# Kernel optimization log

Hardware: AMD Instinct MI355X
Metric: run time of the kernel (lower is better)

Reference implementation:

```python
import jax, jax.numpy as jnp
import numpy as np

NEG_SLOPE = 0.01  # torch nn.LeakyReLU default

N_NODES = 100000
N_EDGES = 1000000
D_FEAT = 64


def setup_inputs() -> dict:
    key = jax.random.key(0)
    ks = jax.random.split(key, 8)
    x = jax.random.normal(ks[0], (N_NODES, D_FEAT), dtype=jnp.float32)
    src = jax.random.randint(ks[1], (N_EDGES,), 0, N_NODES, dtype=jnp.int64 if jax.config.jax_enable_x64 else jnp.int32)
    dst = jax.random.randint(ks[2], (N_EDGES,), 0, N_NODES, dtype=jnp.int64 if jax.config.jax_enable_x64 else jnp.int32)
    s = 1.0 / np.sqrt(D_FEAT)
    W1 = jax.random.normal(ks[3], (D_FEAT, 64), dtype=jnp.float32) * s
    b1 = jnp.zeros((64,), dtype=jnp.float32)
    W2 = jax.random.normal(ks[4], (64, 64), dtype=jnp.float32) * s
    b2 = jnp.zeros((64,), dtype=jnp.float32)
    Wc = jax.random.normal(ks[5], (64, 2), dtype=jnp.float32) * s
    bc = jnp.zeros((2,), dtype=jnp.float32)
    return {"x": x, "src": src, "dst": dst, "W1": W1, "b1": b1,
            "W2": W2, "b2": b2, "Wc": Wc, "bc": bc}


def _graph_conv(x, src, dst, W, b, out_deg_isqrt, in_deg_isqrt, n_nodes):
    # DGL GraphConv, norm='both': h_v = ( sum_{u->v} x_u / sqrt(d_out(u)) ) / sqrt(d_in(v)) @ W + b
    # (in_feats <= out_feats here, so aggregate first then transform, matching DGL order)
    h = x * out_deg_isqrt[:, None]          # [N, d] scale by source out-degree
    msg = h[src]                            # [E, d] gather
    agg = jax.ops.segment_sum(msg, dst, num_segments=n_nodes)  # [N, d] scatter-add
    agg = agg * in_deg_isqrt[:, None]
    return agg @ W + b


def reference(x, src, dst, W1, b1, W2, b2, Wc, bc):
    n = x.shape[0]
    ones_e = jnp.ones(src.shape[0], dtype=x.dtype)
    out_deg = jnp.clip(jax.ops.segment_sum(ones_e, src, num_segments=n), 1.0)
    in_deg = jnp.clip(jax.ops.segment_sum(ones_e, dst, num_segments=n), 1.0)
    out_isqrt = out_deg ** -0.5
    in_isqrt = in_deg ** -0.5

    h = _graph_conv(x, src, dst, W1, b1, out_isqrt, in_isqrt, n)
    h = jax.nn.leaky_relu(h, NEG_SLOPE)
    h = _graph_conv(h, src, dst, W2, b2, out_isqrt, in_isqrt, n)
    h = jax.nn.leaky_relu(h, NEG_SLOPE)
    return h @ Wc + bc  # prediction=True -> linear classifier
```

## Files before the change

### kernel.cpp

```cpp
#include <hip/hip_runtime.h>


typedef __attribute__((ext_vector_type(8))) short short8;
typedef __attribute__((ext_vector_type(4))) float f32x4;

#define NPB 256
#define SEG 64
#define BSH 9
#define BW  512

__device__ __forceinline__ float b2f(unsigned short u) {
    return __uint_as_float(((unsigned int)u) << 16);
}
__device__ __forceinline__ unsigned short f2b(float f) {
    unsigned int i = __float_as_uint(f);
    unsigned int r = (i + 0x7FFFu + ((i >> 16) & 1u)) >> 16;
    return (unsigned short)r;
}

__global__ __launch_bounds__(1024) void count_kernel(
    const int* __restrict__ src, const int* __restrict__ dst,
    int* __restrict__ cntD, int* __restrict__ cntS, int e, int chunk) {
    __shared__ int hD[256], hS[256];
    int t = threadIdx.x, pb = blockIdx.x;
    if (t < 256) { hD[t] = 0; hS[t] = 0; }
    __syncthreads();
    int e0 = pb * chunk, e1 = min(e, e0 + chunk);
    for (int i = e0 + 4 * t; i + 3 < e1; i += 4096) {
        int4 d4 = *(const int4*)(dst + i);
        int4 s4 = *(const int4*)(src + i);
        atomicAdd(&hD[d4.x >> BSH], 1);
        atomicAdd(&hD[d4.y >> BSH], 1);
        atomicAdd(&hD[d4.z >> BSH], 1);
        atomicAdd(&hD[d4.w >> BSH], 1);
        atomicAdd(&hS[s4.x >> BSH], 1);
        atomicAdd(&hS[s4.y >> BSH], 1);
        atomicAdd(&hS[s4.z >> BSH], 1);
        atomicAdd(&hS[s4.w >> BSH], 1);
    }
    int tb0 = e0 + ((e1 - e0) & ~3);
    for (int i = tb0 + t; i < e1; i += 1024) {
        atomicAdd(&hD[dst[i] >> BSH], 1);
        atomicAdd(&hS[src[i] >> BSH], 1);
    }
    __syncthreads();
    if (t < 256) {
        cntD[t * NPB + pb] = hD[t];
        cntS[t * NPB + pb] = hS[t];
    }
}

__global__ __launch_bounds__(1024) void scanmat_kernel(int* __restrict__ cntD,
                                                       int* __restrict__ cntS) {
    int* a = (blockIdx.x == 0) ? cntD : cntS;
    int4* a4 = (int4*)a;
    __shared__ int s[1024];
    int t = threadIdx.x;
    int4 v[SEG / 4];
    int sum = 0;
#pragma unroll
    for (int j = 0; j < SEG / 4; j++) {
        v[j] = a4[t * (SEG / 4) + j];
        sum += v[j].x + v[j].y + v[j].z + v[j].w;
    }
    s[t] = sum;
    __syncthreads();
    for (int d = 1; d < 1024; d <<= 1) {
        int x = (t >= d) ? s[t - d] : 0;
        __syncthreads();
        s[t] += x;
        __syncthreads();
    }
    int run = s[t] - sum;
#pragma unroll
    for (int j = 0; j < SEG / 4; j++) {
        int p0 = run;
        int p1 = p0 + v[j].x;
        int p2 = p1 + v[j].y;
        int p3 = p2 + v[j].z;
        run = p3 + v[j].w;
        a4[t * (SEG / 4) + j] = make_int4(p0, p1, p2, p3);
    }
}

__global__ __launch_bounds__(1024) void part_kernel(
    const int* __restrict__ src, const int* __restrict__ dst,
    const int* __restrict__ cntD, const int* __restrict__ cntS,
    unsigned int* __restrict__ ebuf, unsigned short* __restrict__ sbuf,
    int e, int chunk) {
    __shared__ int cD[256], cS[256];
    int t = threadIdx.x, pb = blockIdx.x;
    if (t < 256) {
        cD[t] = cntD[t * NPB + pb];
        cS[t] = cntS[t * NPB + pb];
    }
    __syncthreads();
    int e0 = pb * chunk, e1 = min(e, e0 + chunk);
    for (int i = e0 + 4 * t; i + 3 < e1; i += 4096) {
        int4 d4 = *(const int4*)(dst + i);
        int4 s4 = *(const int4*)(src + i);
#pragma unroll
        for (int k = 0; k < 4; k++) {
            int s_ = (k == 0) ? s4.x : (k == 1) ? s4.y : (k == 2) ? s4.z : s4.w;
            int d_ = (k == 0) ? d4.x : (k == 1) ? d4.y : (k == 2) ? d4.z : d4.w;
            int pd = atomicAdd(&cD[d_ >> BSH], 1);
            ebuf[pd] = ((unsigned int)s_ << BSH) | (unsigned int)(d_ & (BW - 1));
            int ps_ = atomicAdd(&cS[s_ >> BSH], 1);
            sbuf[ps_] = (unsigned short)(s_ & (BW - 1));
        }
    }
    int tb0 = e0 + ((e1 - e0) & ~3);
    for (int i = tb0 + t; i < e1; i += 1024) {
        int s_ = src[i], d_ = dst[i];
        int pd = atomicAdd(&cD[d_ >> BSH], 1);
        ebuf[pd] = ((unsigned int)s_ << BSH) | (unsigned int)(d_ & (BW - 1));
        int ps_ = atomicAdd(&cS[s_ >> BSH], 1);
        sbuf[ps_] = (unsigned short)(s_ & (BW - 1));
    }
}

__global__ __launch_bounds__(256) void bucket_kernel(
    const unsigned int* __restrict__ ebuf, const unsigned short* __restrict__ sbuf,
    const int* __restrict__ cntD, const int* __restrict__ cntS,
    int* __restrict__ row, float* __restrict__ ii, float* __restrict__ oi,
    int* __restrict__ csr, int n, int e) {
    __shared__ int cnt[BW], cur[BW], ocnt[BW], ps[256];
    int t = threadIdx.x, b = blockIdx.x;
    int v0 = b << BSH;
    int eb0 = cntD[b * NPB], eb1 = cntD[(b + 1) * NPB];
    int sb0 = cntS[b * NPB], sb1 = cntS[(b + 1) * NPB];
    cnt[t] = 0; cnt[t + 256] = 0;
    ocnt[t] = 0; ocnt[t + 256] = 0;
    __syncthreads();
    for (int i = eb0 + t; i < eb1; i += 256)
        atomicAdd(&cnt[ebuf[i] & (BW - 1)], 1);
    for (int i = sb0 + t; i < sb1; i += 256)
        atomicAdd(&ocnt[sbuf[i]], 1);
    __syncthreads();
    int c0 = cnt[2 * t], c1 = cnt[2 * t + 1];
    int pair = c0 + c1;
    ps[t] = pair;
    __syncthreads();
    for (int d = 1; d < 256; d <<= 1) {
        int x = (t >= d) ? ps[t - d] : 0;
        __syncthreads();
        ps[t] += x;
        __syncthreads();
    }
    int excl = ps[t] - pair;
    cur[2 * t] = excl;
    cur[2 * t + 1] = excl + c0;
    int v = v0 + 2 * t;
    if (v < n) {
        row[v] = eb0 + excl;
        ii[v] = rsqrtf((float)max(c0, 1));
    }
    if (v + 1 < n) {
        row[v + 1] = eb0 + excl + c0;
        ii[v + 1] = rsqrtf((float)max(c1, 1));
    }
    if (b == 0 && t == 0) row[n] = e;
    for (int j = t; j < BW; j += 256) {
        int vv = v0 + j;
        if (vv < n) oi[vv] = rsqrtf((float)max(ocnt[j], 1));
    }
    __syncthreads();
    for (int i = eb0 + t; i < eb1; i += 256) {
        unsigned int p = ebuf[i];
        int r = atomicAdd(&cur[p & (BW - 1)], 1);
        csr[eb0 + r] = (int)(p >> BSH);
    }
}

__global__ __launch_bounds__(256) void xconv_kernel(
    const float4* __restrict__ x4, const float* __restrict__ oi,
    ushort4* __restrict__ xb, int total4) {
    int stride = gridDim.x * blockDim.x;
    for (int i = blockIdx.x * blockDim.x + threadIdx.x; i < total4; i += stride) {
        float s = oi[i >> 4];
        float4 val = x4[i];
        xb[i] = make_ushort4(f2b(val.x * s), f2b(val.y * s),
                             f2b(val.z * s), f2b(val.w * s));
    }
}

template <bool FINAL>
__global__ __launch_bounds__(256) void fused_kernel(
    const short8* __restrict__ featb, const int* __restrict__ row,
    const int* __restrict__ csr, const float* __restrict__ ii,
    const float* __restrict__ oi,
    const float* __restrict__ W, const float* __restrict__ bias,
    const float* __restrict__ Wc, const float* __restrict__ bcl,
    void* __restrict__ out, int n, int nwaves) {
    __shared__ short8 tile[4][16 * 9];
    int lane = threadIdx.x & 63;
    int o = lane >> 3, s = lane & 7;
    int m15 = lane & 15, quad = lane >> 4;
    short8* tl = tile[threadIdx.x >> 6];
    int wid = blockIdx.x * (blockDim.x >> 6) + (threadIdx.x >> 6);
    int ngroups = (n + 15) >> 4;

    short8 bf[4][2];
#pragma unroll
    for (int nt = 0; nt < 4; nt++)
#pragma unroll
        for (int kk = 0; kk < 2; kk++)
#pragma unroll
            for (int j = 0; j < 8; j++)
                bf[nt][kk][j] = (short)f2b(W[(kk * 32 + quad * 8 + j) * 64 + nt * 16 + m15]);

    float bias_r[4];
#pragma unroll
    for (int nt = 0; nt < 4; nt++) bias_r[nt] = bias[nt * 16 + m15];

    float wc_r[4][2];
    float bc0 = 0.f, bc1 = 0.f;
    if constexpr (FINAL) {
#pragma unroll
        for (int nt = 0; nt < 4; nt++) {
            wc_r[nt][0] = Wc[(nt * 16 + m15) * 2];
            wc_r[nt][1] = Wc[(nt * 16 + m15) * 2 + 1];
        }
        bc0 = bcl[0];
        bc1 = bcl[1];
    }

    for (int g = wid; g < ngroups; g += nwaves) {
        int rbase = g << 4;

#pragma unroll
        for (int p = 0; p < 2; p++) {
            int v = rbase + p * 8 + o;
            bool valid = v < n;
            int base = 0, cnt = 0;
            if (valid) { base = row[v]; cnt = row[v + 1] - base; }
            float a[8];
#pragma unroll
            for (int k = 0; k < 8; k++) a[k] = 0.f;
            int j = 0;
            for (; j + 3 < cnt; j += 4) {
                int u[4];
#pragma unroll
                for (int k = 0; k < 4; k++) u[k] = csr[base + j + k];
#pragma unroll
                for (int k = 0; k < 4; k++) {
                    short8 f = featb[(size_t)u[k] * 8 + s];
#pragma unroll
                    for (int m = 0; m < 8; m++)
                        a[m] += b2f((unsigned short)f[m]);
                }
            }
            for (; j < cnt; j++) {
                short8 f = featb[(size_t)csr[base + j] * 8 + s];
#pragma unroll
                for (int m = 0; m < 8; m++)
                    a[m] += b2f((unsigned short)f[m]);
            }
            float iiv = valid ? ii[v] : 0.f;
            short8 r;
#pragma unroll
            for (int m = 0; m < 8; m++) r[m] = (short)f2b(a[m] * iiv);
            tl[(p * 8 + o) * 9 + s] = r;
        }

        short8 af0 = tl[m15 * 9 + quad];
        short8 af1 = tl[m15 * 9 + 4 + quad];

        f32x4 acc[4];
#pragma unroll
        for (int nt = 0; nt < 4; nt++) {
            f32x4 z = {0.f, 0.f, 0.f, 0.f};
            z = __builtin_amdgcn_mfma_f32_16x16x32_bf16(af0, bf[nt][0], z, 0, 0, 0);
            z = __builtin_amdgcn_mfma_f32_16x16x32_bf16(af1, bf[nt][1], z, 0, 0, 0);
            acc[nt] = z;
        }

        if constexpr (!FINAL) {
#pragma unroll
            for (int r = 0; r < 4; r++) {
                int vr = rbase + quad * 4 + r;
                float os = (vr < n) ? oi[vr] : 0.f;
#pragma unroll
                for (int nt = 0; nt < 4; nt++) {
                    float ov = acc[nt][r] + bias_r[nt];
                    ov = (ov > 0.f) ? ov : 0.01f * ov;
                    if (vr < n)
                        ((unsigned short*)out)[(size_t)vr * 64 + nt * 16 + m15] = f2b(ov * os);
                }
            }
        } else {
#pragma unroll
            for (int r = 0; r < 4; r++) {
                float p0 = 0.f, p1 = 0.f;
#pragma unroll
                for (int nt = 0; nt < 4; nt++) {
                    float ov = acc[nt][r] + bias_r[nt];
                    ov = (ov > 0.f) ? ov : 0.01f * ov;
                    p0 = fmaf(ov, wc_r[nt][0], p0);
                    p1 = fmaf(ov, wc_r[nt][1], p1);
                }
#pragma unroll
                for (int off = 1; off < 16; off <<= 1) {
                    p0 += __shfl_xor(p0, off);
                    p1 += __shfl_xor(p1, off);
                }
                int vr = rbase + quad * 4 + r;
                if (m15 == 0 && vr < n)
                    ((float2*)out)[vr] = make_float2(p0 + bc0, p1 + bc1);
            }
        }
    }
}

extern "C" void kernel_launch(void* const* d_in, const int* in_sizes, int n_in,
                              void* d_out, int out_size, void* d_ws, size_t ws_size,
                              hipStream_t stream) {
    const float* x  = (const float*)d_in[0];
    const int* src  = (const int*)d_in[1];
    const int* dst  = (const int*)d_in[2];
    const float* W1 = (const float*)d_in[3];
    const float* b1 = (const float*)d_in[4];
    const float* W2 = (const float*)d_in[5];
    const float* b2 = (const float*)d_in[6];
    const float* Wc = (const float*)d_in[7];
    const float* bc = (const float*)d_in[8];
    int n = in_sizes[0] / 64;
    int e = in_sizes[1];
    int total = n * 64;
    int nbuck = (n + BW - 1) >> BSH;

    char* ws = (char*)d_ws;
    size_t off = 0;
    auto take = [&](size_t bytes) -> char* {
        char* p = ws + off;
        off = (off + bytes + 255) & ~(size_t)255;
        return p;
    };
    int* cntD = (int*)take(256 * NPB * 4);
    int* cntS = (int*)take(256 * NPB * 4);
    unsigned int* ebuf = (unsigned int*)take((size_t)e * 4);
    unsigned short* sbuf = (unsigned short*)take((size_t)e * 2);
    int* row  = (int*)take((size_t)(n + 1) * 4);
    int* csr  = (int*)take((size_t)e * 4);
    float* oi = (float*)take((size_t)n * 4);
    float* ii = (float*)take((size_t)n * 4);
    unsigned short* xb  = (unsigned short*)take((size_t)total * 2);
    unsigned short* h1b = (unsigned short*)take((size_t)total * 2);

    int chunk = (((e + NPB - 1) / NPB) + 3) & ~3;

    count_kernel<<<NPB, 1024, 0, stream>>>(src, dst, cntD, cntS, e, chunk);
    scanmat_kernel<<<2, 1024, 0, stream>>>(cntD, cntS);
    part_kernel<<<NPB, 1024, 0, stream>>>(src, dst, cntD, cntS, ebuf, sbuf, e, chunk);
    bucket_kernel<<<nbuck, 256, 0, stream>>>(ebuf, sbuf, cntD, cntS,
                                             row, ii, oi, csr, n, e);
    xconv_kernel<<<2048, 256, 0, stream>>>((const float4*)x, oi, (ushort4*)xb,
                                           n * 16);

    const int fblocks = 1568;
    const int fwaves = fblocks * (256 / 64);

    fused_kernel<false><<<fblocks, 256, 0, stream>>>((const short8*)xb, row, csr, ii, oi,
                                                     W1, b1, nullptr, nullptr, h1b, n, fwaves);
    fused_kernel<true><<<fblocks, 256, 0, stream>>>((const short8*)h1b, row, csr, ii, nullptr,
                                                    W2, b2, Wc, bc, d_out, n, fwaves);
}
```

Before: 207.4 us.

## Pad CSR rows to multiples of four with a zero dummy node and vectorise the gather

Result: faster. 196.8 us (-5.1%).

```diff
diff --git a/kernel.cpp b/kernel.cpp
--- a/kernel.cpp
+++ b/kernel.cpp
@@ -16,6 +16,17 @@
     unsigned int i = __float_as_uint(f);
     unsigned int r = (i + 0x7FFFu + ((i >> 16) & 1u)) >> 16;
     return (unsigned short)r;
+}
+
+__device__ __forceinline__ void acc8(float* a, short8 f) {
+    int4 d = *(int4*)&f;
+#pragma unroll
+    for (int q = 0; q < 4; q++) {
+        unsigned int dw = (unsigned int)((q == 0) ? d.x : (q == 1) ? d.y
+                                       : (q == 2) ? d.z : d.w);
+        a[2 * q]     += __uint_as_float(dw << 16);
+        a[2 * q + 1] += __uint_as_float(dw & 0xFFFF0000u);
+    }
 }
 
 __global__ __launch_bounds__(1024) void count_kernel(
@@ -122,13 +133,15 @@
 __global__ __launch_bounds__(256) void bucket_kernel(
     const unsigned int* __restrict__ ebuf, const unsigned short* __restrict__ sbuf,
     const int* __restrict__ cntD, const int* __restrict__ cntS,
-    int* __restrict__ row, float* __restrict__ ii, float* __restrict__ oi,
+    int* __restrict__ row, int* __restrict__ lenp,
+    float* __restrict__ ii, float* __restrict__ oi,
     int* __restrict__ csr, int n, int e) {
     __shared__ int cnt[BW], cur[BW], ocnt[BW], ps[256];
     int t = threadIdx.x, b = blockIdx.x;
     int v0 = b << BSH;
     int eb0 = cntD[b * NPB], eb1 = cntD[(b + 1) * NPB];
     int sb0 = cntS[b * NPB], sb1 = cntS[(b + 1) * NPB];
+    int pbase = ((eb0 + 3) & ~3) + (v0 << 2);
     cnt[t] = 0; cnt[t + 256] = 0;
     ocnt[t] = 0; ocnt[t + 256] = 0;
     __syncthreads();
@@ -138,8 +151,9 @@
         atomicAdd(&ocnt[sbuf[i]], 1);
     __syncthreads();
     int c0 = cnt[2 * t], c1 = cnt[2 * t + 1];
-    int pair = c0 + c1;
-    ps[t] = pair;
+    int p0 = (c0 + 3) & ~3, p1 = (c1 + 3) & ~3;
+    int ppair = p0 + p1;
+    ps[t] = ppair;
     __syncthreads();
     for (int d = 1; d < 256; d <<= 1) {
         int x = (t >= d) ? ps[t - d] : 0;
@@ -147,19 +161,20 @@
         ps[t] += x;
         __syncthreads();
     }
-    int excl = ps[t] - pair;
-    cur[2 * t] = excl;
-    cur[2 * t + 1] = excl + c0;
+    int pexcl = ps[t] - ppair;
+    cur[2 * t] = pexcl;
+    cur[2 * t + 1] = pexcl + p0;
     int v = v0 + 2 * t;
     if (v < n) {
-        row[v] = eb0 + excl;
+        row[v] = pbase + pexcl;
+        lenp[v] = p0;
         ii[v] = rsqrtf((float)max(c0, 1));
     }
     if (v + 1 < n) {
-        row[v + 1] = eb0 + excl + c0;
+        row[v + 1] = pbase + pexcl + p0;
+        lenp[v + 1] = p1;
         ii[v + 1] = rsqrtf((float)max(c1, 1));
     }
-    if (b == 0 && t == 0) row[n] = e;
     for (int j = t; j < BW; j += 256) {
         int vv = v0 + j;
         if (vv < n) oi[vv] = rsqrtf((float)max(ocnt[j], 1));
@@ -168,27 +183,36 @@
     for (int i = eb0 + t; i < eb1; i += 256) {
         unsigned int p = ebuf[i];
         int r = atomicAdd(&cur[p & (BW - 1)], 1);
-        csr[eb0 + r] = (int)(p >> BSH);
-    }
+        csr[pbase + r] = (int)(p >> BSH);
+    }
+    if (v < n)
+        for (int k = c0; k < p0; k++) csr[pbase + pexcl + k] = n;
+    if (v + 1 < n)
+        for (int k = c1; k < p1; k++) csr[pbase + pexcl + p0 + k] = n;
 }
 
 __global__ __launch_bounds__(256) void xconv_kernel(
     const float4* __restrict__ x4, const float* __restrict__ oi,
-    ushort4* __restrict__ xb, int total4) {
+    ushort4* __restrict__ xb, ushort4* __restrict__ h1b4, int total4) {
+    int idx = blockIdx.x * blockDim.x + threadIdx.x;
     int stride = gridDim.x * blockDim.x;
-    for (int i = blockIdx.x * blockDim.x + threadIdx.x; i < total4; i += stride) {
+    for (int i = idx; i < total4; i += stride) {
         float s = oi[i >> 4];
         float4 val = x4[i];
         xb[i] = make_ushort4(f2b(val.x * s), f2b(val.y * s),
                              f2b(val.z * s), f2b(val.w * s));
     }
+    if (idx < 16) {
+        xb[total4 + idx] = make_ushort4(0, 0, 0, 0);
+        h1b4[total4 + idx] = make_ushort4(0, 0, 0, 0);
+    }
 }
 
 template <bool FINAL>
 __global__ __launch_bounds__(256) void fused_kernel(
     const short8* __restrict__ featb, const int* __restrict__ row,
-    const int* __restrict__ csr, const float* __restrict__ ii,
-    const float* __restrict__ oi,
+    const int* __restrict__ lenp, const int* __restrict__ csr,
+    const float* __restrict__ ii, const float* __restrict__ oi,
     const float* __restrict__ W, const float* __restrict__ bias,
     const float* __restrict__ Wc, const float* __restrict__ bcl,
     void* __restrict__ out, int n, int nwaves) {
@@ -232,29 +256,33 @@
         for (int p = 0; p < 2; p++) {
             int v = rbase + p * 8 + o;
             bool valid = v < n;
-            int base = 0, cnt = 0;
-            if (valid) { base = row[v]; cnt = row[v + 1] - base; }
+            int base = 0, pc = 0;
+            if (valid) { base = row[v]; pc = lenp[v]; }
             float a[8];
 #pragma unroll
             for (int k = 0; k < 8; k++) a[k] = 0.f;
             int j = 0;
-            for (; j + 3 < cnt; j += 4) {
-                int u[4];
-#pragma unroll
-                for (int k = 0; k < 4; k++) u[k] = csr[base + j + k];
-#pragma unroll
-                for (int k = 0; k < 4; k++) {
-                    short8 f = featb[(size_t)u[k] * 8 + s];
-#pragma unroll
-                    for (int m = 0; m < 8; m++)
-                        a[m] += b2f((unsigned short)f[m]);
-                }
+            for (; j + 7 < pc; j += 8) {
+                int4 u0 = *(const int4*)(csr + base + j);
+                int4 u1 = *(const int4*)(csr + base + j + 4);
+                short8 f0 = featb[(size_t)u0.x * 8 + s];
+                short8 f1 = featb[(size_t)u0.y * 8 + s];
+                short8 f2 = featb[(size_t)u0.z * 8 + s];
+                short8 f3 = featb[(size_t)u0.w * 8 + s];
+                short8 f4 = featb[(size_t)u1.x * 8 + s];
+                short8 f5 = featb[(size_t)u1.y * 8 + s];
+                short8 f6 = featb[(size_t)u1.z * 8 + s];
+                short8 f7 = featb[(size_t)u1.w * 8 + s];
+                acc8(a, f0); acc8(a, f1); acc8(a, f2); acc8(a, f3);
+                acc8(a, f4); acc8(a, f5); acc8(a, f6); acc8(a, f7);
             }
-            for (; j < cnt; j++) {
-                short8 f = featb[(size_t)csr[base + j] * 8 + s];
-#pragma unroll
-                for (int m = 0; m < 8; m++)
-                    a[m] += b2f((unsigned short)f[m]);
+            if (j < pc) {
+                int4 u0 = *(const int4*)(csr + base + j);
+                short8 f0 = featb[(size_t)u0.x * 8 + s];
+                short8 f1 = featb[(size_t)u0.y * 8 + s];
+                short8 f2 = featb[(size_t)u0.z * 8 + s];
+                short8 f3 = featb[(size_t)u0.w * 8 + s];
+                acc8(a, f0); acc8(a, f1); acc8(a, f2); acc8(a, f3);
             }
             float iiv = valid ? ii[v] : 0.f;
             short8 r;
@@ -341,11 +369,12 @@
     unsigned int* ebuf = (unsigned int*)take((size_t)e * 4);
     unsigned short* sbuf = (unsigned short*)take((size_t)e * 2);
     int* row  = (int*)take((size_t)(n + 1) * 4);
-    int* csr  = (int*)take((size_t)e * 4);
+    int* lenp = (int*)take((size_t)n * 4);
+    int* csr  = (int*)take(((size_t)e + 4 * (size_t)nbuck * BW + 16) * 4);
     float* oi = (float*)take((size_t)n * 4);
     float* ii = (float*)take((size_t)n * 4);
-    unsigned short* xb  = (unsigned short*)take((size_t)total * 2);
-    unsigned short* h1b = (unsigned short*)take((size_t)total * 2);
+    unsigned short* xb  = (unsigned short*)take((size_t)(total + 64) * 2);
+    unsigned short* h1b = (unsigned short*)take((size_t)(total + 64) * 2);
 
     int chunk = (((e + NPB - 1) / NPB) + 3) & ~3;
 
@@ -353,15 +382,17 @@
     scanmat_kernel<<<2, 1024, 0, stream>>>(cntD, cntS);
     part_kernel<<<NPB, 1024, 0, stream>>>(src, dst, cntD, cntS, ebuf, sbuf, e, chunk);
     bucket_kernel<<<nbuck, 256, 0, stream>>>(ebuf, sbuf, cntD, cntS,
-                                             row, ii, oi, csr, n, e);
+                                             row, lenp, ii, oi, csr, n, e);
     xconv_kernel<<<2048, 256, 0, stream>>>((const float4*)x, oi, (ushort4*)xb,
-                                           n * 16);
+                                           (ushort4*)h1b, n * 16);
 
     const int fblocks = 1568;
     const int fwaves = fblocks * (256 / 64);
 
-    fused_kernel<false><<<fblocks, 256, 0, stream>>>((const short8*)xb, row, csr, ii, oi,
-                                                     W1, b1, nullptr, nullptr, h1b, n, fwaves);
-    fused_kernel<true><<<fblocks, 256, 0, stream>>>((const short8*)h1b, row, csr, ii, nullptr,
-                                                    W2, b2, Wc, bc, d_out, n, fwaves);
-}
+    fused_kernel<false><<<fblocks, 256, 0, stream>>>((const short8*)xb, row, lenp, csr,
+                                                     ii, oi, W1, b1, nullptr, nullptr,
+                                                     h1b, n, fwaves);
+    fused_kernel<true><<<fblocks, 256, 0, stream>>>((const short8*)h1b, row, lenp, csr,
+                                                    ii, nullptr, W2, b2, Wc, bc,
+                                                    d_out, n, fwaves);
+}
```
